# Optimization experiments

Hardware: AMD Instinct MI355X
Metric: run time of the kernel (lower is better)

## Reference

```python
import jax, jax.numpy as jnp
import numpy as np

B = 8        # number of point clouds
P = 2048     # points per cloud
N = B * P
DIN = 128    # input feature dim
K = 32       # max_neighbors
R = 0.2      # ball-query radius
H = 256      # MLP hidden
DOUT = 256   # MLP out


def setup_inputs() -> dict:
    key = jax.random.key(0)
    k1, k2, k3, k4 = jax.random.split(key, 4)
    pos = jax.random.uniform(k1, (N, 3), dtype=jnp.float32)
    x = jax.random.normal(k2, (N, DIN), dtype=jnp.float32)
    batch = jnp.repeat(jnp.arange(B, dtype=jnp.int64), P)
    W1 = jax.random.normal(k3, (DIN + 3, H), dtype=jnp.float32) / np.sqrt(DIN + 3)
    b1 = jnp.zeros((H,), dtype=jnp.float32)
    W2 = jax.random.normal(k4, (H, DOUT), dtype=jnp.float32) / np.sqrt(H)
    b2 = jnp.zeros((DOUT,), dtype=jnp.float32)
    return {"x": x, "pos": pos, "batch": batch,
            "W1": W1, "b1": b1, "W2": W2, "b2": b2}


def reference(x, pos, batch, W1, b1, W2, b2):
    # Equal-size clouds (batch = repeat(arange(B), P)), so reshape keeps
    # the per-cloud structure; cross-cloud pairs are never formed.
    posb = pos.reshape(B, P, 3)
    xb = x.reshape(B, P, DIN)

    # Pairwise squared distances within each cloud: [B, P, P]
    n2 = jnp.sum(posb * posb, axis=-1)
    d2 = n2[:, :, None] + n2[:, None, :] - 2.0 * jnp.einsum('bik,bjk->bij', posb, posb)
    within = d2 <= R * R  # self included (d2[i,i] ~ 0)

    # radius() keeps the first max_neighbors in index order: take the K
    # smallest source indices among valid ones (invalid -> sentinel P).
    jidx = jnp.arange(P, dtype=jnp.int32)
    keys = jnp.where(within, jidx[None, None, :], P)          # [B, P, P]
    negtop, _ = jax.lax.top_k(-keys, K)                       # K smallest keys
    j = -negtop                                               # [B, P, K]
    ok = j < P
    j = jnp.where(ok, j, 0)

    gather = jax.vmap(lambda a, idx: a[idx])                  # per-cloud gather
    x_j = gather(xb, j)                                       # [B, P, K, DIN]
    pos_j = gather(posb, j)                                   # [B, P, K, 3]
    rel = pos_j - posb[:, :, None, :]                         # pos_j - pos_i

    msg = jnp.concatenate([x_j, rel], axis=-1)                # [B, P, K, DIN+3]
    h = jax.nn.relu(jnp.einsum('bpkf,fh->bpkh', msg, W1) + b1)
    h = jax.nn.relu(jnp.einsum('bpkh,ho->bpko', h, W2) + b2)

    # max aggregation over neighbors (every point has itself as neighbor)
    h = jnp.where(ok[..., None], h, -jnp.inf)
    out = jnp.max(h, axis=2).reshape(N, DOUT)
    return out, pos, batch
```

## Files before the change

### kernel.cpp

```cpp
#include <hip/hip_runtime.h>
#include <hip/hip_bf16.h>

#define NPTS   16384
#define PPC    2048
#define DINF   128
#define KNB    32
#define HID    256
#define DOUTF  256

typedef __bf16 bf16x8 __attribute__((ext_vector_type(8)));
typedef __bf16 bf16x4 __attribute__((ext_vector_type(4)));
typedef float  f32x4  __attribute__((ext_vector_type(4)));

#define WS_XBF_OFF   1277952
#define WS_XBF_END   5472256

static __device__ __forceinline__ unsigned short bf16bits(float f) {
    __hip_bfloat16 h = __float2bfloat16(f);
    return *reinterpret_cast<unsigned short*>(&h);
}

__global__ __launch_bounds__(256) void neigh_kernel(
    const float* __restrict__ pos,
    unsigned short* __restrict__ idx,
    unsigned char* __restrict__ cnt)
{
    __shared__ __align__(16) float4 sp[PPC];
    __shared__ unsigned short lists[4][64][KNB];
    __shared__ unsigned char  scnt[4][64];

    const int tid = threadIdx.x;
    const int p0  = blockIdx.x * 64;
    const int cb  = (p0 / PPC) * PPC;

    for (int t = tid; t < PPC; t += 256) {
        const float x = pos[(size_t)(cb + t) * 3 + 0];
        const float y = pos[(size_t)(cb + t) * 3 + 1];
        const float z = pos[(size_t)(cb + t) * 3 + 2];
        const float n2 = __fadd_rn(__fadd_rn(__fmul_rn(x, x), __fmul_rn(y, y)), __fmul_rn(z, z));
        sp[t] = make_float4(x, y, z, n2);
    }
    __syncthreads();

    const int seg = tid >> 6;
    const int p   = tid & 63;
    const float4 pi = sp[p0 - cb + p];

    int c = 0;
    const int jb = seg * (PPC / 4);
    for (int jj = 0; jj < PPC / 4; ++jj) {
        const int j = jb + jj;
        const float4 pj = sp[j];
        const float dot = __fadd_rn(__fadd_rn(__fmul_rn(pi.z, pj.z), __fmul_rn(pi.y, pj.y)),
                                    __fmul_rn(pi.x, pj.x));
        const float d2  = __fsub_rn(__fadd_rn(pi.w, pj.w), __fmul_rn(2.0f, dot));
        if (d2 <= 0.04f && c < KNB) { lists[seg][p][c] = (unsigned short)j; ++c; }
    }
    scnt[seg][p] = (unsigned char)c;
    __syncthreads();

    if (tid < 64) {
        const int point = p0 + tid;
        unsigned short* op = idx + (size_t)point * KNB;
        int k = 0;
        for (int s = 0; s < 4; ++s) {
            const int cc = scnt[s][tid];
            for (int r = 0; r < cc && k < KNB; ++r) op[k++] = lists[s][tid][r];
        }
        cnt[point] = (unsigned char)k;
        for (; k < KNB; ++k) op[k] = 0;
    }
}

__global__ __launch_bounds__(256) void aux_kernel(
    const float* __restrict__ W1, const float* __restrict__ W2,
    const float* __restrict__ pos, const float* __restrict__ x,
    unsigned short* __restrict__ w1s, unsigned short* __restrict__ w2s,
    unsigned short* __restrict__ xbf,
    float* __restrict__ outpos, float* __restrict__ outbat,
    int do_tail, int do_xbf)
{
    const int gid = blockIdx.x * 256 + threadIdx.x;
    if (gid < 5 * 1024) {
        const int ks = gid >> 10, rem = gid & 1023, nt = rem >> 6, lane = rem & 63;
        const int n  = nt * 16 + (lane & 15);
        const int k0 = ks * 32 + ((lane >> 4) * 8);
        unsigned int u[4];
        #pragma unroll
        for (int q = 0; q < 4; ++q) {
            const int ka = k0 + 2 * q, kb = ka + 1;
            const unsigned int lo = (ka < 131) ? (unsigned int)bf16bits(W1[(size_t)ka * HID + n]) : 0u;
            const unsigned int hi = (kb < 131) ? (unsigned int)bf16bits(W1[(size_t)kb * HID + n]) : 0u;
            u[q] = lo | (hi << 16);
        }
        reinterpret_cast<uint4*>(w1s)[gid] = make_uint4(u[0], u[1], u[2], u[3]);
    } else if (gid < 13312) {
        const int t  = gid - 5120;
        const int ks = t >> 10, rem = t & 1023, nt = rem >> 6, lane = rem & 63;
        const int n  = nt * 16 + (lane & 15);
        const int k0 = ks * 32 + ((lane >> 4) * 8);
        unsigned int u[4];
        #pragma unroll
        for (int q = 0; q < 4; ++q) {
            const unsigned int lo = (unsigned int)bf16bits(W2[(size_t)(k0 + 2 * q) * DOUTF + n]);
            const unsigned int hi = (unsigned int)bf16bits(W2[(size_t)(k0 + 2 * q + 1) * DOUTF + n]);
            u[q] = lo | (hi << 16);
        }
        reinterpret_cast<uint4*>(w2s)[t] = make_uint4(u[0], u[1], u[2], u[3]);
    } else if (gid < 13312 + NPTS * 3) {
        if (do_tail) { const int t = gid - 13312; outpos[t] = pos[t]; }
    } else if (gid < 13312 + NPTS * 3 + NPTS) {
        if (do_tail) { const int t = gid - (13312 + NPTS * 3); outbat[t] = (float)(t >> 11); }
    } else {
        const int t = gid - (13312 + NPTS * 3 + NPTS);
        if (do_xbf && t < NPTS * DINF / 8) {
            const float4 a = reinterpret_cast<const float4*>(x)[t * 2];
            const float4 b = reinterpret_cast<const float4*>(x)[t * 2 + 1];
            uint4 v;
            v.x = (unsigned int)bf16bits(a.x) | ((unsigned int)bf16bits(a.y) << 16);
            v.y = (unsigned int)bf16bits(a.z) | ((unsigned int)bf16bits(a.w) << 16);
            v.z = (unsigned int)bf16bits(b.x) | ((unsigned int)bf16bits(b.y) << 16);
            v.w = (unsigned int)bf16bits(b.z) | ((unsigned int)bf16bits(b.w) << 16);
            reinterpret_cast<uint4*>(xbf)[t] = v;
        }
    }
}

#define MSG_STRIDE 168
#define HST        264

template <int XBF>
__global__ __launch_bounds__(512, 4) void sa_kernel_t(
    const float* __restrict__ x,
    const unsigned short* __restrict__ xbf,
    const float* __restrict__ pos,
    const unsigned short* __restrict__ idx,
    const unsigned char*  __restrict__ cnt,
    const unsigned short* __restrict__ w1s,
    const unsigned short* __restrict__ w2s,
    const float* __restrict__ b1,
    const float* __restrict__ b2,
    float* __restrict__ out)
{
    __shared__ __align__(16) unsigned short msg[128 * MSG_STRIDE];
    __shared__ __align__(16) __bf16 hsh[64 * HST];

    const int tid   = threadIdx.x;
    const int pbase = blockIdx.x * 4;
    const int cb    = (pbase >> 11) << 11;

    #pragma unroll
    for (int it = 0; it < 4; ++it) {
        const int task  = it * 512 + tid;
        const int r     = task >> 4;
        const int sg    = task & 15;
        const int point = pbase + (r >> 5);
        const int slot  = r & 31;
        const int j     = idx[point * KNB + slot];
        uint4 v;
        if (XBF) {
            v = *reinterpret_cast<const uint4*>(xbf + (size_t)(cb + j) * DINF + sg * 8);
        } else {
            const float* xf = x + (size_t)(cb + j) * DINF + sg * 8;
            const float4 pa = reinterpret_cast<const float4*>(xf)[0];
            const float4 pb = reinterpret_cast<const float4*>(xf)[1];
            v.x = (unsigned int)bf16bits(pa.x) | ((unsigned int)bf16bits(pa.y) << 16);
            v.y = (unsigned int)bf16bits(pa.z) | ((unsigned int)bf16bits(pa.w) << 16);
            v.z = (unsigned int)bf16bits(pb.x) | ((unsigned int)bf16bits(pb.y) << 16);
            v.w = (unsigned int)bf16bits(pb.z) | ((unsigned int)bf16bits(pb.w) << 16);
        }
        *reinterpret_cast<uint4*>(&msg[r * MSG_STRIDE + sg * 8]) = v;
    }
    if (tid < 128) {
        const int r     = tid;
        const int point = pbase + (r >> 5);
        const int slot  = r & 31;
        const int j     = idx[point * KNB + slot];
        const float rx = pos[(size_t)(cb + j) * 3 + 0] - pos[(size_t)point * 3 + 0];
        const float ry = pos[(size_t)(cb + j) * 3 + 1] - pos[(size_t)point * 3 + 1];
        const float rz = pos[(size_t)(cb + j) * 3 + 2] - pos[(size_t)point * 3 + 2];
        uint4 vr;
        vr.x = (unsigned int)bf16bits(rx) | ((unsigned int)bf16bits(ry) << 16);
        vr.y = (unsigned int)bf16bits(rz);
        vr.z = 0u; vr.w = 0u;
        const uint4 z = make_uint4(0u, 0u, 0u, 0u);
        *reinterpret_cast<uint4*>(&msg[r * MSG_STRIDE + 128]) = vr;
        *reinterpret_cast<uint4*>(&msg[r * MSG_STRIDE + 136]) = z;
        *reinterpret_cast<uint4*>(&msg[r * MSG_STRIDE + 144]) = z;
        *reinterpret_cast<uint4*>(&msg[r * MSG_STRIDE + 152]) = z;
    }

    const int w    = tid >> 6;
    const int lane = tid & 63;
    const int quad = lane >> 4;
    const int l15  = lane & 15;

    bf16x8 wf1[5][2];
    #pragma unroll
    for (int ks = 0; ks < 5; ++ks)
        #pragma unroll
        for (int nt = 0; nt < 2; ++nt)
            wf1[ks][nt] = *reinterpret_cast<const bf16x8*>(
                w1s + (size_t)((ks * 16 + (w * 2 + nt)) * 64 + lane) * 8);
    float bb1[2][4];
    #pragma unroll
    for (int nt = 0; nt < 2; ++nt) {
        const float4 bv = *reinterpret_cast<const float4*>(b1 + (w * 2 + nt) * 16 + quad * 4);
        bb1[nt][0] = bv.x; bb1[nt][1] = bv.y; bb1[nt][2] = bv.z; bb1[nt][3] = bv.w;
    }
    float bb2[2];
    #pragma unroll
    for (int nt = 0; nt < 2; ++nt) bb2[nt] = b2[(w * 2 + nt) * 16 + l15];
    int myc[4];
    #pragma unroll
    for (int p = 0; p < 4; ++p) {
        int c = cnt[pbase + p];
        myc[p] = (c > KNB) ? KNB : c;
    }
    __syncthreads();

    const f32x4 fz = {0.f, 0.f, 0.f, 0.f};

    for (int ph = 0; ph < 2; ++ph) {
        #pragma unroll
        for (int mt = 0; mt < 4; ++mt) {
            f32x4 a1[2] = {fz, fz};
            #pragma unroll
            for (int ks = 0; ks < 5; ++ks) {
                const bf16x8 av = *reinterpret_cast<const bf16x8*>(
                    msg + ((ph * 4 + mt) * 16 + l15) * MSG_STRIDE + ks * 32 + quad * 8);
                #pragma unroll
                for (int nt = 0; nt < 2; ++nt)
                    a1[nt] = __builtin_amdgcn_mfma_f32_16x16x32_bf16(wf1[ks][nt], av, a1[nt], 0, 0, 0);
            }
            #pragma unroll
            for (int nt = 0; nt < 2; ++nt) {
                bf16x4 hv4;
                #pragma unroll
                for (int rg = 0; rg < 4; ++rg)
                    hv4[rg] = (__bf16)fmaxf(a1[nt][rg] + bb1[nt][rg], 0.f);
                *reinterpret_cast<bf16x4*>(
                    &hsh[(mt * 16 + l15) * HST + (w * 2 + nt) * 16 + quad * 4]) = hv4;
            }
        }
        __syncthreads();

        f32x4 acc2[4][2];
        #pragma unroll
        for (int mt = 0; mt < 4; ++mt)
            #pragma unroll
            for (int nt = 0; nt < 2; ++nt) acc2[mt][nt] = fz;

        #pragma unroll
        for (int ks = 0; ks < 8; ++ks) {
            bf16x8 wf2[2];
            #pragma unroll
            for (int nt = 0; nt < 2; ++nt)
                wf2[nt] = *reinterpret_cast<const bf16x8*>(
                    w2s + (size_t)((ks * 16 + (w * 2 + nt)) * 64 + lane) * 8);
            #pragma unroll
            for (int mt = 0; mt < 4; ++mt) {
                const bf16x8 hv = *reinterpret_cast<const bf16x8*>(
                    hsh + (mt * 16 + l15) * HST + ks * 32 + quad * 8);
                #pragma unroll
                for (int nt = 0; nt < 2; ++nt)
                    acc2[mt][nt] = __builtin_amdgcn_mfma_f32_16x16x32_bf16(hv, wf2[nt], acc2[mt][nt], 0, 0, 0);
            }
        }

        #pragma unroll
        for (int nt = 0; nt < 2; ++nt) {
            const int col = (w * 2 + nt) * 16 + l15;
            const float bv = bb2[nt];
            #pragma unroll
            for (int p = 0; p < 2; ++p) {
                const int point = pbase + ph * 2 + p;
                const int mc = myc[ph * 2 + p];
                float m = 0.f;
                #pragma unroll
                for (int hh = 0; hh < 2; ++hh) {
                    const int mt = 2 * p + hh;
                    #pragma unroll
                    for (int rg = 0; rg < 4; ++rg) {
                        const int slot = hh * 16 + quad * 4 + rg;
                        const float v = fmaxf(acc2[mt][nt][rg] + bv, 0.f);
                        if (slot < mc) m = fmaxf(m, v);
                    }
                }
                m = fmaxf(m, __shfl_xor(m, 16, 64));
                m = fmaxf(m, __shfl_xor(m, 32, 64));
                if (lane < 16) out[(size_t)point * DOUTF + col] = m;
            }
        }
        __syncthreads();
    }
}

extern "C" void kernel_launch(void* const* d_in, const int* in_sizes, int n_in,
                              void* d_out, int out_size, void* d_ws, size_t ws_size,
                              hipStream_t stream)
{
    const float *x = nullptr, *pos = nullptr, *W1 = nullptr, *W2 = nullptr;
    const float *b1 = nullptr, *b2 = nullptr;
    int nbias = 0;
    for (int i = 0; i < n_in && i < 16; ++i) {
        switch (in_sizes[i]) {
            case NPTS * DINF: x   = (const float*)d_in[i]; break;
            case NPTS * 3:    pos = (const float*)d_in[i]; break;
            case 131 * HID:   W1  = (const float*)d_in[i]; break;
            case HID * DOUTF: W2  = (const float*)d_in[i]; break;
            case 256:         if (nbias == 0) b1 = (const float*)d_in[i];
                              else            b2 = (const float*)d_in[i];
                              ++nbias; break;
            default: break;
        }
    }
    if (!x)   x   = (const float*)d_in[0];
    if (!pos) pos = (const float*)d_in[1];
    if (!W1)  W1  = (const float*)d_in[3];
    if (!b1)  b1  = (const float*)d_in[4];
    if (!W2)  W2  = (const float*)d_in[5];
    if (!b2)  b2  = (const float*)d_in[6];

    char* ws = (char*)d_ws;
    unsigned short* idx = (unsigned short*)(ws + 0);
    unsigned char*  cnt = (unsigned char*)(ws + 1048576);
    unsigned short* w1s = (unsigned short*)(ws + 1064960);
    unsigned short* w2s = (unsigned short*)(ws + 1146880);
    unsigned short* xbf = (unsigned short*)(ws + WS_XBF_OFF);

    const int use_xbf  = (ws_size >= (size_t)WS_XBF_END) ? 1 : 0;
    const int do_tail  = (out_size >= NPTS * DOUTF + NPTS * 3 + NPTS) ? 1 : 0;

    float* out    = (float*)d_out;
    float* outpos = out + (size_t)NPTS * DOUTF;
    float* outbat = outpos + (size_t)NPTS * 3;

    hipLaunchKernelGGL(neigh_kernel, dim3(NPTS / 64), dim3(256), 0, stream, pos, idx, cnt);
    hipLaunchKernelGGL(aux_kernel,   dim3(1332),      dim3(256), 0, stream,
                       W1, W2, pos, x, w1s, w2s, xbf, outpos, outbat, do_tail, use_xbf);
    if (use_xbf) {
        hipLaunchKernelGGL((sa_kernel_t<1>), dim3(NPTS / 4), dim3(512), 0, stream,
                           x, xbf, pos, idx, cnt, w1s, w2s, b1, b2, out);
    } else {
        hipLaunchKernelGGL((sa_kernel_t<0>), dim3(NPTS / 4), dim3(512), 0, stream,
                           x, xbf, pos, idx, cnt, w1s, w2s, b1, b2, out);
    }
}
```

Before: 228.0 us.

## Precompute x·W1 per point once and gather it instead of per-edge first-layer GEMM

Uses the linearity of the first MLP layer to compute y = x·W1[:128] once per point with a new GEMM kernel. The edge kernel then gathers fp32 y rows per neighbour and adds only the rel-pos contribution through a single MFMA k-step. This removes the 32x redundant first-layer work, in exchange for a large fp32 workspace and heavier gather traffic. It also widens the neighbour-search kernel to 8 segments of 512 threads. The new path runs only when the workspace is large enough, otherwise it falls back to the old kernels.

```diff
diff --git a/kernel.cpp b/kernel.cpp
--- a/kernel.cpp
+++ b/kernel.cpp
@@ -14,26 +14,28 @@
 
 #define WS_XBF_OFF   1277952
 #define WS_XBF_END   5472256
+#define WS_Y_OFF     1277952
+#define WS_Y_END     18055168
 
 static __device__ __forceinline__ unsigned short bf16bits(float f) {
     __hip_bfloat16 h = __float2bfloat16(f);
     return *reinterpret_cast<unsigned short*>(&h);
 }
 
-__global__ __launch_bounds__(256) void neigh_kernel(
+__global__ __launch_bounds__(512) void neigh_kernel(
     const float* __restrict__ pos,
     unsigned short* __restrict__ idx,
     unsigned char* __restrict__ cnt)
 {
     __shared__ __align__(16) float4 sp[PPC];
-    __shared__ unsigned short lists[4][64][KNB];
-    __shared__ unsigned char  scnt[4][64];
+    __shared__ unsigned short lists[8][64][KNB];
+    __shared__ unsigned char  scnt[8][64];
 
     const int tid = threadIdx.x;
     const int p0  = blockIdx.x * 64;
     const int cb  = (p0 / PPC) * PPC;
 
-    for (int t = tid; t < PPC; t += 256) {
+    for (int t = tid; t < PPC; t += 512) {
         const float x = pos[(size_t)(cb + t) * 3 + 0];
         const float y = pos[(size_t)(cb + t) * 3 + 1];
         const float z = pos[(size_t)(cb + t) * 3 + 2];
@@ -47,8 +49,8 @@
     const float4 pi = sp[p0 - cb + p];
 
     int c = 0;
-    const int jb = seg * (PPC / 4);
-    for (int jj = 0; jj < PPC / 4; ++jj) {
+    const int jb = seg * (PPC / 8);
+    for (int jj = 0; jj < PPC / 8; ++jj) {
         const int j = jb + jj;
         const float4 pj = sp[j];
         const float dot = __fadd_rn(__fadd_rn(__fmul_rn(pi.z, pj.z), __fmul_rn(pi.y, pj.y)),
@@ -63,7 +65,7 @@
         const int point = p0 + tid;
         unsigned short* op = idx + (size_t)point * KNB;
         int k = 0;
-        for (int s = 0; s < 4; ++s) {
+        for (int s = 0; s < 8; ++s) {
             const int cc = scnt[s][tid];
             for (int r = 0; r < cc && k < KNB; ++r) op[k++] = lists[s][tid][r];
         }
@@ -126,8 +128,227 @@
     }
 }
 
+#define XS_STRIDE 136
+
+__global__ __launch_bounds__(512, 4) void gemm_y_kernel(
+    const float* __restrict__ x,
+    const unsigned short* __restrict__ w1s,
+    float* __restrict__ y)
+{
+    __shared__ __align__(16) unsigned short xs[128 * XS_STRIDE];
+
+    const int tid = threadIdx.x;
+    const int rb  = blockIdx.x * 128;
+
+    #pragma unroll
+    for (int it = 0; it < 4; ++it) {
+        const int task = it * 512 + tid;
+        const int r    = task >> 4;
+        const int sg   = task & 15;
+        const float* xf = x + (size_t)(rb + r) * DINF + sg * 8;
+        const float4 pa = reinterpret_cast<const float4*>(xf)[0];
+        const float4 pb = reinterpret_cast<const float4*>(xf)[1];
+        uint4 v;
+        v.x = (unsigned int)bf16bits(pa.x) | ((unsigned int)bf16bits(pa.y) << 16);
+        v.y = (unsigned int)bf16bits(pa.z) | ((unsigned int)bf16bits(pa.w) << 16);
+        v.z = (unsigned int)bf16bits(pb.x) | ((unsigned int)bf16bits(pb.y) << 16);
+        v.w = (unsigned int)bf16bits(pb.z) | ((unsigned int)bf16bits(pb.w) << 16);
+        *reinterpret_cast<uint4*>(&xs[r * XS_STRIDE + sg * 8]) = v;
+    }
+    __syncthreads();
+
+    const int w    = tid >> 6;
+    const int lane = tid & 63;
+    const int quad = lane >> 4;
+    const int l15  = lane & 15;
+
+    bf16x8 wf[4][2];
+    #pragma unroll
+    for (int ks = 0; ks < 4; ++ks)
+        #pragma unroll
+        for (int nt = 0; nt < 2; ++nt)
+            wf[ks][nt] = *reinterpret_cast<const bf16x8*>(
+                w1s + (size_t)((ks * 16 + (w * 2 + nt)) * 64 + lane) * 8);
+
+    const f32x4 fz = {0.f, 0.f, 0.f, 0.f};
+    #pragma unroll
+    for (int mt = 0; mt < 8; ++mt) {
+        f32x4 a[2] = {fz, fz};
+        #pragma unroll
+        for (int ks = 0; ks < 4; ++ks) {
+            const bf16x8 av = *reinterpret_cast<const bf16x8*>(
+                xs + (mt * 16 + l15) * XS_STRIDE + ks * 32 + quad * 8);
+            #pragma unroll
+            for (int nt = 0; nt < 2; ++nt)
+                a[nt] = __builtin_amdgcn_mfma_f32_16x16x32_bf16(wf[ks][nt], av, a[nt], 0, 0, 0);
+        }
+        #pragma unroll
+        for (int nt = 0; nt < 2; ++nt)
+            *reinterpret_cast<f32x4*>(
+                y + (size_t)(rb + mt * 16 + l15) * DOUTF + (w * 2 + nt) * 16 + quad * 4) = a[nt];
+    }
+}
+
+#define RST 40
+#define HST 264
+
+__global__ __launch_bounds__(512, 6) void sa_kernel_y(
+    const float* __restrict__ y,
+    const float* __restrict__ pos,
+    const unsigned short* __restrict__ idx,
+    const unsigned char*  __restrict__ cnt,
+    const unsigned short* __restrict__ w1s,
+    const unsigned short* __restrict__ w2s,
+    const float* __restrict__ b1,
+    const float* __restrict__ b2,
+    float* __restrict__ out)
+{
+    __shared__ __align__(16) unsigned short relds[128 * RST];
+    __shared__ __align__(16) __bf16 hsh[64 * HST];
+
+    const int tid   = threadIdx.x;
+    const int pbase = blockIdx.x * 4;
+    const int cb    = (pbase >> 11) << 11;
+
+    if (tid < 128) {
+        const int r     = tid;
+        const int point = pbase + (r >> 5);
+        const int slot  = r & 31;
+        const int j     = idx[point * KNB + slot];
+        const float rx = pos[(size_t)(cb + j) * 3 + 0] - pos[(size_t)point * 3 + 0];
+        const float ry = pos[(size_t)(cb + j) * 3 + 1] - pos[(size_t)point * 3 + 1];
+        const float rz = pos[(size_t)(cb + j) * 3 + 2] - pos[(size_t)point * 3 + 2];
+        uint4 vr;
+        vr.x = (unsigned int)bf16bits(rx) | ((unsigned int)bf16bits(ry) << 16);
+        vr.y = (unsigned int)bf16bits(rz);
+        vr.z = 0u; vr.w = 0u;
+        const uint4 z = make_uint4(0u, 0u, 0u, 0u);
+        *reinterpret_cast<uint4*>(&relds[r * RST + 0])  = vr;
+        *reinterpret_cast<uint4*>(&relds[r * RST + 8])  = z;
+        *reinterpret_cast<uint4*>(&relds[r * RST + 16]) = z;
+        *reinterpret_cast<uint4*>(&relds[r * RST + 24]) = z;
+    }
+
+    const int w    = tid >> 6;
+    const int lane = tid & 63;
+    const int quad = lane >> 4;
+    const int l15  = lane & 15;
+
+    float bb2[2];
+    #pragma unroll
+    for (int nt = 0; nt < 2; ++nt) bb2[nt] = b2[(w * 2 + nt) * 16 + l15];
+    int myc[4];
+    #pragma unroll
+    for (int p = 0; p < 4; ++p) {
+        int c = cnt[pbase + p];
+        myc[p] = (c > KNB) ? KNB : c;
+    }
+    __syncthreads();
+
+    const f32x4 fz = {0.f, 0.f, 0.f, 0.f};
+
+    for (int ph = 0; ph < 2; ++ph) {
+        bf16x8 wf1rel[2];
+        #pragma unroll
+        for (int nt = 0; nt < 2; ++nt)
+            wf1rel[nt] = *reinterpret_cast<const bf16x8*>(
+                w1s + (size_t)((4 * 16 + (w * 2 + nt)) * 64 + lane) * 8);
+        float bb1[2][4];
+        #pragma unroll
+        for (int nt = 0; nt < 2; ++nt) {
+            const float4 bv = *reinterpret_cast<const float4*>(b1 + (w * 2 + nt) * 16 + quad * 4);
+            bb1[nt][0] = bv.x; bb1[nt][1] = bv.y; bb1[nt][2] = bv.z; bb1[nt][3] = bv.w;
+        }
+        int jrow[4];
+        #pragma unroll
+        for (int mt = 0; mt < 4; ++mt) {
+            const int row = ph * 64 + mt * 16 + l15;
+            jrow[mt] = idx[(pbase + (row >> 5)) * KNB + (row & 31)];
+        }
+
+        f32x4 ycur[2], ynxt[2];
+        #pragma unroll
+        for (int nt = 0; nt < 2; ++nt)
+            ycur[nt] = *reinterpret_cast<const f32x4*>(
+                y + (size_t)(cb + jrow[0]) * DOUTF + (w * 2 + nt) * 16 + quad * 4);
+        #pragma unroll
+        for (int mt = 0; mt < 4; ++mt) {
+            if (mt < 3) {
+                #pragma unroll
+                for (int nt = 0; nt < 2; ++nt)
+                    ynxt[nt] = *reinterpret_cast<const f32x4*>(
+                        y + (size_t)(cb + jrow[mt + 1]) * DOUTF + (w * 2 + nt) * 16 + quad * 4);
+            }
+            const bf16x8 av = *reinterpret_cast<const bf16x8*>(
+                relds + (ph * 64 + mt * 16 + l15) * RST + quad * 8);
+            #pragma unroll
+            for (int nt = 0; nt < 2; ++nt) {
+                const f32x4 a1 = __builtin_amdgcn_mfma_f32_16x16x32_bf16(
+                    wf1rel[nt], av, ycur[nt], 0, 0, 0);
+                bf16x4 hv4;
+                #pragma unroll
+                for (int rg = 0; rg < 4; ++rg)
+                    hv4[rg] = (__bf16)fmaxf(a1[rg] + bb1[nt][rg], 0.f);
+                *reinterpret_cast<bf16x4*>(
+                    &hsh[(mt * 16 + l15) * HST + (w * 2 + nt) * 16 + quad * 4]) = hv4;
+            }
+            #pragma unroll
+            for (int nt = 0; nt < 2; ++nt) ycur[nt] = ynxt[nt];
+        }
+        __syncthreads();
+
+        f32x4 acc2[4][2];
+        #pragma unroll
+        for (int mt = 0; mt < 4; ++mt)
+            #pragma unroll
+            for (int nt = 0; nt < 2; ++nt) acc2[mt][nt] = fz;
+
+        #pragma unroll
+        for (int ks = 0; ks < 8; ++ks) {
+            bf16x8 wf2[2];
+            #pragma unroll
+            for (int nt = 0; nt < 2; ++nt)
+                wf2[nt] = *reinterpret_cast<const bf16x8*>(
+                    w2s + (size_t)((ks * 16 + (w * 2 + nt)) * 64 + lane) * 8);
+            #pragma unroll
+            for (int mt = 0; mt < 4; ++mt) {
+                const bf16x8 hv = *reinterpret_cast<const bf16x8*>(
+                    hsh + (mt * 16 + l15) * HST + ks * 32 + quad * 8);
+                #pragma unroll
+                for (int nt = 0; nt < 2; ++nt)
+                    acc2[mt][nt] = __builtin_amdgcn_mfma_f32_16x16x32_bf16(hv, wf2[nt], acc2[mt][nt], 0, 0, 0);
+            }
+        }
+
+        #pragma unroll
+        for (int nt = 0; nt < 2; ++nt) {
+            const int col = (w * 2 + nt) * 16 + l15;
+            const float bv = bb2[nt];
+            #pragma unroll
+            for (int p = 0; p < 2; ++p) {
+                const int point = pbase + ph * 2 + p;
+                const int mc = myc[ph * 2 + p];
+                float m = 0.f;
+                #pragma unroll
+                for (int hh = 0; hh < 2; ++hh) {
+                    const int mt = 2 * p + hh;
+                    #pragma unroll
+                    for (int rg = 0; rg < 4; ++rg) {
+                        const int slot = hh * 16 + quad * 4 + rg;
+                        const float v = fmaxf(acc2[mt][nt][rg] + bv, 0.f);
+                        if (slot < mc) m = fmaxf(m, v);
+                    }
+                }
+                m = fmaxf(m, __shfl_xor(m, 16, 64));
+                m = fmaxf(m, __shfl_xor(m, 32, 64));
+                if (lane < 16) out[(size_t)point * DOUTF + col] = m;
+            }
+        }
+        __syncthreads();
+    }
+}
+
 #define MSG_STRIDE 168
-#define HST        264
 
 template <int XBF>
 __global__ __launch_bounds__(512, 4) void sa_kernel_t(
@@ -328,18 +549,24 @@
     unsigned short* w1s = (unsigned short*)(ws + 1064960);
     unsigned short* w2s = (unsigned short*)(ws + 1146880);
     unsigned short* xbf = (unsigned short*)(ws + WS_XBF_OFF);
-
-    const int use_xbf  = (ws_size >= (size_t)WS_XBF_END) ? 1 : 0;
-    const int do_tail  = (out_size >= NPTS * DOUTF + NPTS * 3 + NPTS) ? 1 : 0;
+    float*          yws = (float*)(ws + WS_Y_OFF);
+
+    const int use_y   = (ws_size >= (size_t)WS_Y_END) ? 1 : 0;
+    const int use_xbf = (!use_y && ws_size >= (size_t)WS_XBF_END) ? 1 : 0;
+    const int do_tail = (out_size >= NPTS * DOUTF + NPTS * 3 + NPTS) ? 1 : 0;
 
     float* out    = (float*)d_out;
     float* outpos = out + (size_t)NPTS * DOUTF;
     float* outbat = outpos + (size_t)NPTS * 3;
 
-    hipLaunchKernelGGL(neigh_kernel, dim3(NPTS / 64), dim3(256), 0, stream, pos, idx, cnt);
+    hipLaunchKernelGGL(neigh_kernel, dim3(NPTS / 64), dim3(512), 0, stream, pos, idx, cnt);
     hipLaunchKernelGGL(aux_kernel,   dim3(1332),      dim3(256), 0, stream,
                        W1, W2, pos, x, w1s, w2s, xbf, outpos, outbat, do_tail, use_xbf);
-    if (use_xbf) {
+    if (use_y) {
+        hipLaunchKernelGGL(gemm_y_kernel, dim3(NPTS / 128), dim3(512), 0, stream, x, w1s, yws);
+        hipLaunchKernelGGL(sa_kernel_y,   dim3(NPTS / 4),   dim3(512), 0, stream,
+                           yws, pos, idx, cnt, w1s, w2s, b1, b2, out);
+    } else if (use_xbf) {
         hipLaunchKernelGGL((sa_kernel_t<1>), dim3(NPTS / 4), dim3(512), 0, stream,
                            x, xbf, pos, idx, cnt, w1s, w2s, b1, b2, out);
     } else {
```

New measurement: 268.5 us. 1.18x slower.

## Split neighbor scan across 8 segments and retile MLP warps as 2x4 grid

Applied to the files above, without the earlier changes.

The neighbor search kernel now uses 512 threads and 8 segments per point, halving each thread's serial scan over the cloud. The fused MLP kernel reassigns its 8 waves from 8 column strips covering all 64 rows to a 2x4 grid, so each wave handles 32 rows by 64 columns. Each wave now streams W1 fragments per k-step instead of holding all of them in registers, and reads half as many LDS rows per k-step. Each wave also reduces a single point per phase and reads its neighbor count directly. The tradeoff is more global or cache weight loads per wave, more registers for the larger accumulator tile, and more shared memory for the neighbor lists.

```diff
diff --git a/kernel.cpp b/kernel.cpp
--- a/kernel.cpp
+++ b/kernel.cpp
@@ -20,20 +20,20 @@
     return *reinterpret_cast<unsigned short*>(&h);
 }
 
-__global__ __launch_bounds__(256) void neigh_kernel(
+__global__ __launch_bounds__(512) void neigh_kernel(
     const float* __restrict__ pos,
     unsigned short* __restrict__ idx,
     unsigned char* __restrict__ cnt)
 {
     __shared__ __align__(16) float4 sp[PPC];
-    __shared__ unsigned short lists[4][64][KNB];
-    __shared__ unsigned char  scnt[4][64];
+    __shared__ unsigned short lists[8][64][KNB];
+    __shared__ unsigned char  scnt[8][64];
 
     const int tid = threadIdx.x;
     const int p0  = blockIdx.x * 64;
     const int cb  = (p0 / PPC) * PPC;
 
-    for (int t = tid; t < PPC; t += 256) {
+    for (int t = tid; t < PPC; t += 512) {
         const float x = pos[(size_t)(cb + t) * 3 + 0];
         const float y = pos[(size_t)(cb + t) * 3 + 1];
         const float z = pos[(size_t)(cb + t) * 3 + 2];
@@ -47,8 +47,8 @@
     const float4 pi = sp[p0 - cb + p];
 
     int c = 0;
-    const int jb = seg * (PPC / 4);
-    for (int jj = 0; jj < PPC / 4; ++jj) {
+    const int jb = seg * (PPC / 8);
+    for (int jj = 0; jj < PPC / 8; ++jj) {
         const int j = jb + jj;
         const float4 pj = sp[j];
         const float dot = __fadd_rn(__fadd_rn(__fmul_rn(pi.z, pj.z), __fmul_rn(pi.y, pj.y)),
@@ -63,7 +63,7 @@
         const int point = p0 + tid;
         unsigned short* op = idx + (size_t)point * KNB;
         int k = 0;
-        for (int s = 0; s < 4; ++s) {
+        for (int s = 0; s < 8; ++s) {
             const int cc = scnt[s][tid];
             for (int r = 0; r < cc && k < KNB; ++r) op[k++] = lists[s][tid][r];
         }
@@ -191,98 +191,100 @@
     }
 
     const int w    = tid >> 6;
+    const int wr   = w >> 2;
+    const int wc   = w & 3;
     const int lane = tid & 63;
     const int quad = lane >> 4;
     const int l15  = lane & 15;
 
-    bf16x8 wf1[5][2];
+    float bb1[4][4];
     #pragma unroll
-    for (int ks = 0; ks < 5; ++ks)
-        #pragma unroll
-        for (int nt = 0; nt < 2; ++nt)
-            wf1[ks][nt] = *reinterpret_cast<const bf16x8*>(
-                w1s + (size_t)((ks * 16 + (w * 2 + nt)) * 64 + lane) * 8);
-    float bb1[2][4];
+    for (int nt = 0; nt < 4; ++nt) {
+        const float4 bv = *reinterpret_cast<const float4*>(b1 + (wc * 4 + nt) * 16 + quad * 4);
+        bb1[nt][0] = bv.x; bb1[nt][1] = bv.y; bb1[nt][2] = bv.z; bb1[nt][3] = bv.w;
+    }
+    float bb2[4];
     #pragma unroll
-    for (int nt = 0; nt < 2; ++nt) {
-        const float4 bv = *reinterpret_cast<const float4*>(b1 + (w * 2 + nt) * 16 + quad * 4);
-        bb1[nt][0] = bv.x; bb1[nt][1] = bv.y; bb1[nt][2] = bv.z; bb1[nt][3] = bv.w;
-    }
-    float bb2[2];
+    for (int nt = 0; nt < 4; ++nt) bb2[nt] = b2[(wc * 4 + nt) * 16 + l15];
+    __syncthreads();
+
+    const f32x4 fz = {0.f, 0.f, 0.f, 0.f};
+
     #pragma unroll
-    for (int nt = 0; nt < 2; ++nt) bb2[nt] = b2[(w * 2 + nt) * 16 + l15];
-    int myc[4];
-    #pragma unroll
-    for (int p = 0; p < 4; ++p) {
-        int c = cnt[pbase + p];
-        myc[p] = (c > KNB) ? KNB : c;
-    }
-    __syncthreads();
-
-    const f32x4 fz = {0.f, 0.f, 0.f, 0.f};
-
     for (int ph = 0; ph < 2; ++ph) {
-        #pragma unroll
-        for (int mt = 0; mt < 4; ++mt) {
-            f32x4 a1[2] = {fz, fz};
-            #pragma unroll
-            for (int ks = 0; ks < 5; ++ks) {
+        f32x4 acc1[2][4];
+        #pragma unroll
+        for (int mt = 0; mt < 2; ++mt)
+            #pragma unroll
+            for (int nt = 0; nt < 4; ++nt) acc1[mt][nt] = fz;
+
+        #pragma unroll
+        for (int ks = 0; ks < 5; ++ks) {
+            bf16x8 w1f[4];
+            #pragma unroll
+            for (int nt = 0; nt < 4; ++nt)
+                w1f[nt] = *reinterpret_cast<const bf16x8*>(
+                    w1s + (size_t)((ks * 16 + (wc * 4 + nt)) * 64 + lane) * 8);
+            #pragma unroll
+            for (int mt = 0; mt < 2; ++mt) {
                 const bf16x8 av = *reinterpret_cast<const bf16x8*>(
-                    msg + ((ph * 4 + mt) * 16 + l15) * MSG_STRIDE + ks * 32 + quad * 8);
+                    msg + (ph * 64 + wr * 32 + mt * 16 + l15) * MSG_STRIDE + ks * 32 + quad * 8);
                 #pragma unroll
-                for (int nt = 0; nt < 2; ++nt)
-                    a1[nt] = __builtin_amdgcn_mfma_f32_16x16x32_bf16(wf1[ks][nt], av, a1[nt], 0, 0, 0);
+                for (int nt = 0; nt < 4; ++nt)
+                    acc1[mt][nt] = __builtin_amdgcn_mfma_f32_16x16x32_bf16(w1f[nt], av, acc1[mt][nt], 0, 0, 0);
             }
-            #pragma unroll
-            for (int nt = 0; nt < 2; ++nt) {
+        }
+        #pragma unroll
+        for (int mt = 0; mt < 2; ++mt) {
+            #pragma unroll
+            for (int nt = 0; nt < 4; ++nt) {
                 bf16x4 hv4;
                 #pragma unroll
                 for (int rg = 0; rg < 4; ++rg)
-                    hv4[rg] = (__bf16)fmaxf(a1[nt][rg] + bb1[nt][rg], 0.f);
+                    hv4[rg] = (__bf16)fmaxf(acc1[mt][nt][rg] + bb1[nt][rg], 0.f);
                 *reinterpret_cast<bf16x4*>(
-                    &hsh[(mt * 16 + l15) * HST + (w * 2 + nt) * 16 + quad * 4]) = hv4;
+                    &hsh[(wr * 32 + mt * 16 + l15) * HST + (wc * 4 + nt) * 16 + quad * 4]) = hv4;
             }
         }
         __syncthreads();
 
-        f32x4 acc2[4][2];
-        #pragma unroll
-        for (int mt = 0; mt < 4; ++mt)
-            #pragma unroll
-            for (int nt = 0; nt < 2; ++nt) acc2[mt][nt] = fz;
+        f32x4 acc2[2][4];
+        #pragma unroll
+        for (int mt = 0; mt < 2; ++mt)
+            #pragma unroll
+            for (int nt = 0; nt < 4; ++nt) acc2[mt][nt] = fz;
 
         #pragma unroll
         for (int ks = 0; ks < 8; ++ks) {
-            bf16x8 wf2[2];
-            #pragma unroll
-            for (int nt = 0; nt < 2; ++nt)
-                wf2[nt] = *reinterpret_cast<const bf16x8*>(
-                    w2s + (size_t)((ks * 16 + (w * 2 + nt)) * 64 + lane) * 8);
-            #pragma unroll
-            for (int mt = 0; mt < 4; ++mt) {
+            bf16x8 w2f[4];
+            #pragma unroll
+            for (int nt = 0; nt < 4; ++nt)
+                w2f[nt] = *reinterpret_cast<const bf16x8*>(
+                    w2s + (size_t)((ks * 16 + (wc * 4 + nt)) * 64 + lane) * 8);
+            #pragma unroll
+            for (int mt = 0; mt < 2; ++mt) {
                 const bf16x8 hv = *reinterpret_cast<const bf16x8*>(
-                    hsh + (mt * 16 + l15) * HST + ks * 32 + quad * 8);
+                    hsh + (wr * 32 + mt * 16 + l15) * HST + ks * 32 + quad * 8);
                 #pragma unroll
-                for (int nt = 0; nt < 2; ++nt)
-                    acc2[mt][nt] = __builtin_amdgcn_mfma_f32_16x16x32_bf16(hv, wf2[nt], acc2[mt][nt], 0, 0, 0);
+                for (int nt = 0; nt < 4; ++nt)
+                    acc2[mt][nt] = __builtin_amdgcn_mfma_f32_16x16x32_bf16(hv, w2f[nt], acc2[mt][nt], 0, 0, 0);
             }
         }
 
-        #pragma unroll
-        for (int nt = 0; nt < 2; ++nt) {
-            const int col = (w * 2 + nt) * 16 + l15;
-            const float bv = bb2[nt];
-            #pragma unroll
-            for (int p = 0; p < 2; ++p) {
-                const int point = pbase + ph * 2 + p;
-                const int mc = myc[ph * 2 + p];
+        {
+            const int point = pbase + ph * 2 + wr;
+            int mc = cnt[point];
+            mc = (mc > KNB) ? KNB : mc;
+            #pragma unroll
+            for (int nt = 0; nt < 4; ++nt) {
+                const int col = (wc * 4 + nt) * 16 + l15;
+                const float bv = bb2[nt];
                 float m = 0.f;
                 #pragma unroll
-                for (int hh = 0; hh < 2; ++hh) {
-                    const int mt = 2 * p + hh;
+                for (int mt = 0; mt < 2; ++mt) {
                     #pragma unroll
                     for (int rg = 0; rg < 4; ++rg) {
-                        const int slot = hh * 16 + quad * 4 + rg;
+                        const int slot = mt * 16 + quad * 4 + rg;
                         const float v = fmaxf(acc2[mt][nt][rg] + bv, 0.f);
                         if (slot < mc) m = fmaxf(m, v);
                     }
@@ -329,14 +331,14 @@
     unsigned short* w2s = (unsigned short*)(ws + 1146880);
     unsigned short* xbf = (unsigned short*)(ws + WS_XBF_OFF);
 
-    const int use_xbf  = (ws_size >= (size_t)WS_XBF_END) ? 1 : 0;
-    const int do_tail  = (out_size >= NPTS * DOUTF + NPTS * 3 + NPTS) ? 1 : 0;
+    const int use_xbf = (ws_size >= (size_t)WS_XBF_END) ? 1 : 0;
+    const int do_tail = (out_size >= NPTS * DOUTF + NPTS * 3 + NPTS) ? 1 : 0;
 
     float* out    = (float*)d_out;
     float* outpos = out + (size_t)NPTS * DOUTF;
     float* outbat = outpos + (size_t)NPTS * 3;
 
-    hipLaunchKernelGGL(neigh_kernel, dim3(NPTS / 64), dim3(256), 0, stream, pos, idx, cnt);
+    hipLaunchKernelGGL(neigh_kernel, dim3(NPTS / 64), dim3(512), 0, stream, pos, idx, cnt);
     hipLaunchKernelGGL(aux_kernel,   dim3(1332),      dim3(256), 0, stream,
                        W1, W2, pos, x, w1s, w2s, xbf, outpos, outbat, do_tail, use_xbf);
     if (use_xbf) {
```

After: 346.4 us. 1.52x slower.
